# Kernel tuning notes

Measured on AMD Instinct MI355X. Metric: run time of the kernel, lower is better.

The kernel has to match this reference:

```python
import jax, jax.numpy as jnp
import numpy as np

E = 64      # embedding_dim
H = 64      # h_dim
MLP = 1024  # mlp_dim (attention hidden)
PRE1 = 512  # mlp_pre_pool hidden
BNK = 1024  # bottleneck_dim
S = 256     # num scenes (equal-size groups replacing seq_start_end)
P = 16      # pedestrians per scene
B = S * P   # total batch of pedestrians
T = 8       # obs_len for vx/vy (only last row used)
EPS = 1e-5  # BatchNorm eps


def _bn(x, g, b, m, v):
    # eval-mode BatchNorm1d over the last (feature) axis
    return (x - m) * jax.lax.rsqrt(v + EPS) * g + b


def setup_inputs() -> dict:
    key = jax.random.key(0)
    ks = jax.random.split(key, 24)
    def n(k, shape, s=1.0):
        return jax.random.normal(k, shape, jnp.float32) * s
    return {
        "h_states": n(ks[0], (1, B, H)),
        "end_pos": n(ks[1], (B, 2)),
        "vx": n(ks[2], (T, B)),
        "vy": n(ks[3], (T, B)),
        "W_sp": n(ks[4], (2, E), 0.05), "b_sp": jnp.zeros((E,), jnp.float32),
        "W_vel": n(ks[5], (2, E), 0.05), "b_vel": jnp.zeros((E,), jnp.float32),
        "Wa1": n(ks[6], (2 * E, MLP), 0.05), "ba1": jnp.zeros((MLP,), jnp.float32),
        "ga1": jnp.ones((MLP,), jnp.float32), "bta1": jnp.zeros((MLP,), jnp.float32),
        "ma1": n(ks[7], (MLP,), 0.1), "va1": jax.random.uniform(ks[8], (MLP,), jnp.float32) + 0.5,
        "Wa2": n(ks[9], (MLP, 1), 0.05), "ba2": jnp.zeros((1,), jnp.float32),
        "ga2": jnp.ones((1,), jnp.float32), "bta2": jnp.zeros((1,), jnp.float32),
        "ma2": n(ks[10], (1,), 0.1), "va2": jax.random.uniform(ks[11], (1,), jnp.float32) + 0.5,
        "Wp1": n(ks[12], (E + H, PRE1), 0.05), "bp1": jnp.zeros((PRE1,), jnp.float32),
        "gp1": jnp.ones((PRE1,), jnp.float32), "btp1": jnp.zeros((PRE1,), jnp.float32),
        "mp1": n(ks[13], (PRE1,), 0.1), "vp1": jax.random.uniform(ks[14], (PRE1,), jnp.float32) + 0.5,
        "Wp2": n(ks[15], (PRE1, BNK), 0.05), "bp2": jnp.zeros((BNK,), jnp.float32),
        "gp2": jnp.ones((BNK,), jnp.float32), "btp2": jnp.zeros((BNK,), jnp.float32),
        "mp2": n(ks[16], (BNK,), 0.1), "vp2": jax.random.uniform(ks[17], (BNK,), jnp.float32) + 0.5,
        "num_scenes": S, "num_ped": P,
    }


def _forward(h_states, end_pos, vx, vy, W_sp, b_sp, W_vel, b_vel,
             Wa1, ba1, ga1, bta1, ma1, va1, Wa2, ba2, ga2, bta2, ma2, va2,
             Wp1, bp1, gp1, btp1, mp1, vp1, Wp2, bp2, gp2, btp2, mp2, vp2,
             num_scenes, num_ped):
    Sn, Pn = num_scenes, num_ped
    h = h_states.reshape(-1, H).reshape(Sn, Pn, H)          # per-scene hidden
    pos = end_pos.reshape(Sn, Pn, 2)
    # rel[s,i,j] = pos[s,j] - pos[s,i]  (repeat vs repeat_interleave in torch)
    rel = pos[:, None, :, :] - pos[:, :, None, :]
    rel_emb = rel @ W_sp + b_sp                              # [S,P,P,E]
    vel = jnp.stack([vx[-1], vy[-1]], axis=-1).reshape(Sn, Pn, 2)
    vel_emb = vel @ W_vel + b_vel                            # [S,P,E], indexed by row i
    vel_emb = jnp.broadcast_to(vel_emb[:, :, None, :], (Sn, Pn, Pn, E))
    att_in = jnp.concatenate([rel_emb, vel_emb], axis=-1)    # [S,P,P,2E]
    a = jax.nn.relu(_bn(att_in @ Wa1 + ba1, ga1, bta1, ma1, va1))
    scores = jax.nn.relu(_bn(a @ Wa2 + ba2, ga2, bta2, ma2, va2))  # [S,P,P,1]
    # torch.softmax(scores, dim=1) on an (N,1) tensor: softmax over the size-1
    # feature axis -> identically 1.0. Reproduced faithfully here.
    w = jax.nn.softmax(scores, axis=-1)
    h_rep = jnp.broadcast_to(h[:, None, :, :], (Sn, Pn, Pn, H))   # h[s,j] per (i,j)
    x = jnp.concatenate([rel_emb, h_rep], axis=-1) * (0.05 * w)   # [S,P,P,E+H]
    y = jax.nn.relu(_bn(x @ Wp1 + bp1, gp1, btp1, mp1, vp1))
    y = jax.nn.relu(_bn(y @ Wp2 + bp2, gp2, btp2, mp2, vp2))      # [S,P,P,BNK]
    pool = jnp.max(y, axis=2)                                     # max over neighbors j
    return pool.reshape(Sn * Pn, BNK)


def reference(h_states, end_pos, vx, vy, W_sp, b_sp, W_vel, b_vel,
              Wa1, ba1, ga1, bta1, ma1, va1, Wa2, ba2, ga2, bta2, ma2, va2,
              Wp1, bp1, gp1, btp1, mp1, vp1, Wp2, bp2, gp2, btp2, mp2, vp2,
              num_scenes, num_ped):
    return _forward(h_states, end_pos, vx, vy, W_sp, b_sp, W_vel, b_vel,
                    Wa1, ba1, ga1, bta1, ma1, va1, Wa2, ba2, ga2, bta2, ma2, va2,
                    Wp1, bp1, gp1, btp1, mp1, vp1, Wp2, bp2, gp2, btp2, mp2, vp2,
                    num_scenes, num_ped)
```

## Files before the change

kernel.cpp:

```cpp
#include <hip/hip_runtime.h>
#include <hip/hip_bf16.h>
#include <stdint.h>
#include <utility>


typedef __bf16 bf16x8 __attribute__((ext_vector_type(8)));
typedef __bf16 bf16x2 __attribute__((ext_vector_type(2)));
typedef float  f32x4  __attribute__((ext_vector_type(4)));
typedef float  f32x2  __attribute__((ext_vector_type(2)));
typedef float  f32x16 __attribute__((ext_vector_type(16)));

#define BP2_OFF 0u
#define BP1_OFF 1048576u
#define MX_OFF  1114112u
#define MY_OFF  1116160u
#define CB_OFF  1118208u
#define SH_OFF  1120256u
#define A2_OFF  1122304u
#define C2_OFF  1126400u

#define Y1_LDS  0
#define HH_LDS  131072
#define LDS_SZ  147456

__device__ __forceinline__ unsigned short f2bf(float f) {
    union { float f; unsigned u; } c; c.f = f;
    unsigned u = c.u;
    return (unsigned short)((u + 0x7fffu + ((u >> 16) & 1u)) >> 16);
}
__device__ __forceinline__ float bfbits2f(unsigned hi) {
    union { unsigned u; float f; } c; c.u = hi; return c.f;
}
__device__ __forceinline__ unsigned pk_bf16(float a, float b) {
#if __has_builtin(__builtin_amdgcn_cvt_pk_bf16_f32)
    bf16x2 p = __builtin_amdgcn_cvt_pk_bf16_f32(a, b);
    union { bf16x2 v; unsigned u; } c; c.v = p; return c.u;
#else
    return (unsigned)f2bf(a) | ((unsigned)f2bf(b) << 16);
#endif
}
__device__ __forceinline__ int y1off(int r, int c16) {
    return r * 1024 + ((c16 ^ (r & 7)) << 4);
}

template<class F, int... Is>
__device__ __forceinline__ void sf_impl(F& f, std::integer_sequence<int, Is...>) {
    (f(std::integral_constant<int, Is>{}), ...);
}
template<int N, class F>
__device__ __forceinline__ void static_for(F&& f) {
    sf_impl(f, std::make_integer_sequence<int, N>{});
}

__global__ __launch_bounds__(256) void prep_pack_kernel(
    const float* __restrict__ Wsp,  const float* __restrict__ bsp,
    const float* __restrict__ Wp1,  const float* __restrict__ bp1,
    const float* __restrict__ gp1,  const float* __restrict__ btp1,
    const float* __restrict__ mp1,  const float* __restrict__ vp1,
    const float* __restrict__ Wp2,  const float* __restrict__ bp2,
    const float* __restrict__ gp2,  const float* __restrict__ btp2,
    const float* __restrict__ mp2,  const float* __restrict__ vp2,
    unsigned char* __restrict__ ws)
{
    __shared__ float tile[32 * 65];
    __shared__ float part[3][4][64];
    const int blk = blockIdx.x, t = threadIdx.x;

    if (blk < 272) {
        const float* src; int ncols, kb, ng;
        if (blk < 256) { kb = blk >> 4; ng = blk & 15; src = Wp2; ncols = 1024; }
        else { int b2 = blk - 256; kb = b2 >> 3; ng = b2 & 7; src = Wp1 + 64 * 512; ncols = 512; }
        const int k0 = kb * 32, n0 = ng * 64;
        #pragma unroll
        for (int it = 0; it < 2; ++it) {
            int c = t + it * 256;
            int r = c >> 4, c4 = c & 15;
            float4 v = *(const float4*)(src + (k0 + r) * ncols + n0 + c4 * 4);
            tile[r * 65 + c4 * 4 + 0] = v.x;
            tile[r * 65 + c4 * 4 + 1] = v.y;
            tile[r * 65 + c4 * 4 + 2] = v.z;
            tile[r * 65 + c4 * 4 + 3] = v.w;
        }
        __syncthreads();
        if (blk < 256) {
            const int l = t & 63, ch = (t >> 6) & 1, kh = t >> 7;
            const int nl = ch * 32 + (l & 31);
            const int kl = kh * 16 + ((l >> 5) & 1) * 8;
            uint4 o;
            o.x = pk_bf16(tile[(kl + 0) * 65 + nl], tile[(kl + 1) * 65 + nl]);
            o.y = pk_bf16(tile[(kl + 2) * 65 + nl], tile[(kl + 3) * 65 + nl]);
            o.z = pk_bf16(tile[(kl + 4) * 65 + nl], tile[(kl + 5) * 65 + nl]);
            o.w = pk_bf16(tile[(kl + 6) * 65 + nl], tile[(kl + 7) * 65 + nl]);
            const int kstep = kb * 2 + kh, ct = ng * 2 + ch;
            ((uint4*)(ws + BP2_OFF))[(kstep * 32 + ct) * 64 + l] = o;
        } else {
            int ntl = t >> 6, l = t & 63;
            int nl = ntl * 16 + (l & 15), kl = (l >> 4) * 8;
            uint4 o;
            o.x = pk_bf16(tile[(kl + 0) * 65 + nl], tile[(kl + 1) * 65 + nl]);
            o.y = pk_bf16(tile[(kl + 2) * 65 + nl], tile[(kl + 3) * 65 + nl]);
            o.z = pk_bf16(tile[(kl + 4) * 65 + nl], tile[(kl + 5) * 65 + nl]);
            o.w = pk_bf16(tile[(kl + 6) * 65 + nl], tile[(kl + 7) * 65 + nl]);
            ((uint4*)(ws + BP1_OFF))[((ng * 4 + ntl) * 2 + kb) * 64 + l] = o;
        }
    } else if (blk < 280) {
        const int kk = t & 63, eq = t >> 6;
        const int k = (blk - 272) * 64 + kk;
        float mx = 0.f, my = 0.f, cb = 0.f;
        #pragma unroll
        for (int e2 = 0; e2 < 16; ++e2) {
            int e = eq * 16 + e2;
            float wv = Wp1[e * 512 + k];
            mx = fmaf(Wsp[e],      wv, mx);
            my = fmaf(Wsp[64 + e], wv, my);
            cb = fmaf(bsp[e],      wv, cb);
        }
        part[0][eq][kk] = mx; part[1][eq][kk] = my; part[2][eq][kk] = cb;
        __syncthreads();
        if (t < 64) {
            const int k2 = (blk - 272) * 64 + t;
            float mxs = part[0][0][t] + part[0][1][t] + part[0][2][t] + part[0][3][t];
            float mys = part[1][0][t] + part[1][1][t] + part[1][2][t] + part[1][3][t];
            float cbs = part[2][0][t] + part[2][1][t] + part[2][2][t] + part[2][3][t];
            float a1 = gp1[k2] * rsqrtf(vp1[k2] + 1e-5f);
            ((float*)(ws + MX_OFF))[k2] = 0.05f * a1 * mxs;
            ((float*)(ws + MY_OFF))[k2] = 0.05f * a1 * mys;
            ((float*)(ws + CB_OFF))[k2] = 0.05f * a1 * cbs + (bp1[k2] - mp1[k2]) * a1 + btp1[k2];
            ((float*)(ws + SH_OFF))[k2] = 0.05f * a1;
        }
    } else {
        int n = (blk - 280) * 256 + t;
        float a = gp2[n] * rsqrtf(vp2[n] + 1e-5f);
        ((float*)(ws + A2_OFF))[n] = a;
        ((float*)(ws + C2_OFF))[n] = btp2[n] + (bp2[n] - mp2[n]) * a;
    }
}

__device__ __forceinline__ void phaseAB(
    unsigned char* smem,
    const float* __restrict__ hst, const float* __restrict__ epos,
    const unsigned char* __restrict__ ws, int s, int ih, int tid)
{
    const int w    = tid >> 6;
    const int l    = tid & 63;
    const int quad = l >> 4;
    const int jl   = l & 15;

    {
        union { unsigned u[4]; bf16x8 v; } afh[2];
        #pragma unroll
        for (int kb = 0; kb < 2; ++kb) {
            const float4* hp = (const float4*)(hst + (s * 16 + jl) * 64 + kb * 32 + quad * 8);
            float4 v0 = hp[0], v1 = hp[1];
            afh[kb].u[0] = pk_bf16(v0.x, v0.y);
            afh[kb].u[1] = pk_bf16(v0.z, v0.w);
            afh[kb].u[2] = pk_bf16(v1.x, v1.y);
            afh[kb].u[3] = pk_bf16(v1.z, v1.w);
        }
        const f32x4 fz = {0.f, 0.f, 0.f, 0.f};
        f32x4 acch[4] = {fz, fz, fz, fz};
        #pragma unroll
        for (int kb = 0; kb < 2; ++kb) {
            #pragma unroll
            for (int ct = 0; ct < 4; ++ct) {
                bf16x8 bfr = *(const bf16x8*)(ws + BP1_OFF + ((((w * 4 + ct) * 2 + kb) * 64 + l) << 4));
                acch[ct] = __builtin_amdgcn_mfma_f32_16x16x32_bf16(afh[kb].v, bfr, acch[ct], 0, 0, 0);
            }
        }
        const float* SHg = (const float*)(ws + SH_OFF);
        const float* CBg = (const float*)(ws + CB_OFF);
        #pragma unroll
        for (int ct = 0; ct < 4; ++ct) {
            int col = (w * 4 + ct) * 16 + jl;
            float sh = SHg[col], cb = CBg[col];
            #pragma unroll
            for (int reg = 0; reg < 4; ++reg) {
                int j = quad * 4 + reg;
                float hv = fmaf(acch[ct][reg], sh, cb);
                *(unsigned short*)(smem + HH_LDS + j * 1024 + col * 2) = f2bf(hv);
            }
        }
    }
    __syncthreads();

    {
        const int i2 = tid >> 8;
        const int j  = (tid >> 4) & 15;
        const int kc = tid & 15;
        float rx[4], ry[4];
        float pjx = epos[s * 32 + j * 2], pjy = epos[s * 32 + j * 2 + 1];
        #pragma unroll
        for (int ii = 0; ii < 4; ++ii) {
            int ig_ = ih * 8 + i2 * 4 + ii;
            rx[ii] = pjx - epos[s * 32 + ig_ * 2];
            ry[ii] = pjy - epos[s * 32 + ig_ * 2 + 1];
        }
        const f32x2 zero2 = {0.f, 0.f};
        #pragma unroll
        for (int kk = 0; kk < 4; ++kk) {
            int c16 = kk * 16 + kc;
            int k = c16 * 8;
            uint4 hh8 = *(const uint4*)(smem + HH_LDS + j * 1024 + k * 2);
            f32x4 mx0 = *(const f32x4*)(ws + MX_OFF + k * 4);
            f32x4 mx1 = *(const f32x4*)(ws + MX_OFF + k * 4 + 16);
            f32x4 my0 = *(const f32x4*)(ws + MY_OFF + k * 4);
            f32x4 my1 = *(const f32x4*)(ws + MY_OFF + k * 4 + 16);
            f32x2 mxp[4] = { {mx0[0],mx0[1]}, {mx0[2],mx0[3]}, {mx1[0],mx1[1]}, {mx1[2],mx1[3]} };
            f32x2 myp[4] = { {my0[0],my0[1]}, {my0[2],my0[3]}, {my1[0],my1[1]}, {my1[2],my1[3]} };
            f32x2 hhp[4];
            hhp[0][0] = bfbits2f(hh8.x << 16); hhp[0][1] = bfbits2f(hh8.x & 0xffff0000u);
            hhp[1][0] = bfbits2f(hh8.y << 16); hhp[1][1] = bfbits2f(hh8.y & 0xffff0000u);
            hhp[2][0] = bfbits2f(hh8.z << 16); hhp[2][1] = bfbits2f(hh8.z & 0xffff0000u);
            hhp[3][0] = bfbits2f(hh8.w << 16); hhp[3][1] = bfbits2f(hh8.w & 0xffff0000u);
            #pragma unroll
            for (int ii = 0; ii < 4; ++ii) {
                f32x2 rx2 = { rx[ii], rx[ii] };
                f32x2 ry2 = { ry[ii], ry[ii] };
                uint4 o;
                unsigned uu[4];
                #pragma unroll
                for (int p = 0; p < 4; ++p) {
                    f32x2 tt = __builtin_elementwise_fma(ry2, myp[p], hhp[p]);
                    tt = __builtin_elementwise_fma(rx2, mxp[p], tt);
                    tt = __builtin_elementwise_max(tt, zero2);
                    uu[p] = pk_bf16(tt[0], tt[1]);
                }
                o.x = uu[0]; o.y = uu[1]; o.z = uu[2]; o.w = uu[3];
                int r = (i2 * 4 + ii) * 16 + j;
                *(uint4*)(smem + Y1_LDS + y1off(r, c16)) = o;
            }
        }
    }
    __syncthreads();
}

__global__ __launch_bounds__(512, 2) void mm2_kernel(
    const float* __restrict__ hst,
    const float* __restrict__ epos,
    const unsigned char* __restrict__ ws,
    float* __restrict__ out)
{
    __shared__ __align__(16) unsigned char smem[LDS_SZ];

    const int s   = blockIdx.x >> 1;
    const int ih  = blockIdx.x & 1;
    const int tid = threadIdx.x;

    phaseAB(smem, hst, epos, ws, s, ih, tid);

    const int w = tid >> 6, l = tid & 63;
    const int lane31 = l & 31;
    const int hi = l >> 5;
    const int sr = lane31 & 7;
    const int rg = w >> 2;
    const int cg = w & 3;
    const float* A2 = (const float*)(ws + A2_OFF);
    const float* C2 = (const float*)(ws + C2_OFF);

    const int av = Y1_LDS + (rg * 64 + lane31) * 1024 + ((hi ^ sr) << 4);
    const unsigned char* bp = ws + BP2_OFF + ((cg * 4) << 10) + (l << 4);

    const f32x16 fz16 = {0.f,0.f,0.f,0.f,0.f,0.f,0.f,0.f,
                         0.f,0.f,0.f,0.f,0.f,0.f,0.f,0.f};
    f32x16 acc[2][4];
    bf16x8 ar[4][2];
    bf16x8 br[3][4];

    #pragma unroll
    for (int rr = 0; rr < 2; ++rr)
        #pragma unroll
        for (int c = 0; c < 4; ++c) acc[rr][c] = fz16;

    auto epilogue = [&](int pass) {
        #pragma unroll
        for (int c = 0; c < 4; ++c) {
            const int col = (pass * 16 + cg * 4 + c) * 32 + lane31;
            const float a2 = A2[col], c2 = C2[col];
            #pragma unroll
            for (int rr = 0; rr < 2; ++rr) {
                float mv[2];
                #pragma unroll
                for (int hg = 0; hg < 2; ++hg) {
                    float v0 = fmaxf(fmaf(acc[rr][c][hg * 8 + 0], a2, c2), 0.f);
                    float v1 = fmaxf(fmaf(acc[rr][c][hg * 8 + 1], a2, c2), 0.f);
                    float v2 = fmaxf(fmaf(acc[rr][c][hg * 8 + 2], a2, c2), 0.f);
                    float v3 = fmaxf(fmaf(acc[rr][c][hg * 8 + 3], a2, c2), 0.f);
                    float v4 = fmaxf(fmaf(acc[rr][c][hg * 8 + 4], a2, c2), 0.f);
                    float v5 = fmaxf(fmaf(acc[rr][c][hg * 8 + 5], a2, c2), 0.f);
                    float v6 = fmaxf(fmaf(acc[rr][c][hg * 8 + 6], a2, c2), 0.f);
                    float v7 = fmaxf(fmaf(acc[rr][c][hg * 8 + 7], a2, c2), 0.f);
                    float m = fmaxf(fmaxf(fmaxf(v0, v1), fmaxf(v2, v3)),
                                    fmaxf(fmaxf(v4, v5), fmaxf(v6, v7)));
                    mv[hg] = fmaxf(m, __shfl_xor(m, 32, 64));
                }
                const int iloc = (rg * 2 + rr) * 2 + hi;
                const float vout = hi ? mv[1] : mv[0];
                const int orow = s * 16 + ih * 8 + iloc;
                __builtin_nontemporal_store(vout, &out[orow * 1024 + col]);
            }
        }
    };

    auto stepG = [&](auto Gc) {
        constexpr int G  = decltype(Gc)::value;
        constexpr int GN = G + 2;
        if constexpr (GN <= 63) {
            constexpr int pn = GN >> 5, kn = GN & 31;
            constexpr int bs = GN % 3, as = GN & 3;
            const unsigned char* b = bp + (pn * 16384 + kn * 32768);
            #pragma unroll
            for (int c = 0; c < 4; ++c)
                br[bs][c] = *(const bf16x8*)(b + c * 1024);
            constexpr int add = (kn >> 2) * 128;
            constexpr int xr  = (kn & 3) << 5;
            ar[as][0] = *(const bf16x8*)(smem + ((av + add) ^ xr));
            ar[as][1] = *(const bf16x8*)(smem + (((av + add) ^ xr) + 32768));
        }
        if constexpr (G == 32 || G == 33)
            asm volatile("s_waitcnt vmcnt(16) lgkmcnt(4)" ::: "memory");
        else if constexpr (G == 62)
            asm volatile("s_waitcnt vmcnt(4) lgkmcnt(2)" ::: "memory");
        else if constexpr (G == 63)
            asm volatile("s_waitcnt vmcnt(0) lgkmcnt(0)" ::: "memory");
        else
            asm volatile("s_waitcnt vmcnt(8) lgkmcnt(4)" ::: "memory");
        __builtin_amdgcn_sched_barrier(0);
        constexpr int as2 = G & 3, bs2 = G % 3;
        #pragma unroll
        for (int c = 0; c < 4; ++c)
            #pragma unroll
            for (int rr = 0; rr < 2; ++rr)
                acc[rr][c] = __builtin_amdgcn_mfma_f32_32x32x16_bf16(
                    ar[as2][rr], br[bs2][c], acc[rr][c], 0, 0, 0);
    };

    #pragma unroll
    for (int g = 0; g < 2; ++g)
        #pragma unroll
        for (int c = 0; c < 4; ++c)
            br[g][c] = *(const bf16x8*)(bp + g * 32768 + c * 1024);
    ar[0][0] = *(const bf16x8*)(smem + av);
    ar[0][1] = *(const bf16x8*)(smem + av + 32768);
    ar[1][0] = *(const bf16x8*)(smem + (av ^ 32));
    ar[1][1] = *(const bf16x8*)(smem + ((av ^ 32) + 32768));

    static_for<32>(stepG);
    __builtin_amdgcn_sched_barrier(0);
    epilogue(0);
    #pragma unroll
    for (int rr = 0; rr < 2; ++rr)
        #pragma unroll
        for (int c = 0; c < 4; ++c) acc[rr][c] = fz16;
    __builtin_amdgcn_sched_barrier(0);
    static_for<32>([&](auto kc) {
        stepG(std::integral_constant<int, decltype(kc)::value + 32>{});
    });
    __builtin_amdgcn_sched_barrier(0);
    epilogue(1);
}

extern "C" void kernel_launch(void* const* d_in, const int* in_sizes, int n_in,
                              void* d_out, int out_size, void* d_ws, size_t ws_size,
                              hipStream_t stream) {
    const float* hst  = (const float*)d_in[0];
    const float* epos = (const float*)d_in[1];
    const float* Wsp  = (const float*)d_in[4];
    const float* bsp  = (const float*)d_in[5];
    const float* Wp1  = (const float*)d_in[20];
    const float* bp1  = (const float*)d_in[21];
    const float* gp1  = (const float*)d_in[22];
    const float* btp1 = (const float*)d_in[23];
    const float* mp1  = (const float*)d_in[24];
    const float* vp1  = (const float*)d_in[25];
    const float* Wp2  = (const float*)d_in[26];
    const float* bp2  = (const float*)d_in[27];
    const float* gp2  = (const float*)d_in[28];
    const float* btp2 = (const float*)d_in[29];
    const float* mp2  = (const float*)d_in[30];
    const float* vp2  = (const float*)d_in[31];
    unsigned char* ws = (unsigned char*)d_ws;
    float* out = (float*)d_out;

    prep_pack_kernel<<<284, 256, 0, stream>>>(Wsp, bsp, Wp1, bp1, gp1, btp1, mp1, vp1,
                                              Wp2, bp2, gp2, btp2, mp2, vp2, ws);
    mm2_kernel<<<512, 512, 0, stream>>>(hst, epos, ws, out);
}
```

Measured before the change: 186.8 us.

## Split each scene into four 4-row blocks of 256 threads instead of two

```diff
diff --git a/kernel.cpp b/kernel.cpp
--- a/kernel.cpp
+++ b/kernel.cpp
@@ -20,8 +20,8 @@
 #define C2_OFF  1126400u
 
 #define Y1_LDS  0
-#define HH_LDS  131072
-#define LDS_SZ  147456
+#define HH_LDS  65536
+#define LDS_SZ  81920
 
 __device__ __forceinline__ unsigned short f2bf(float f) {
     union { float f; unsigned u; } c; c.f = f;
@@ -136,11 +136,17 @@
     }
 }
 
-__device__ __forceinline__ void phaseAB(
-    unsigned char* smem,
-    const float* __restrict__ hst, const float* __restrict__ epos,
-    const unsigned char* __restrict__ ws, int s, int ih, int tid)
+__global__ __launch_bounds__(256, 2) void mm3_kernel(
+    const float* __restrict__ hst,
+    const float* __restrict__ epos,
+    const unsigned char* __restrict__ ws,
+    float* __restrict__ out)
 {
+    __shared__ __align__(16) unsigned char smem[LDS_SZ];
+
+    const int s   = blockIdx.x >> 2;
+    const int q   = blockIdx.x & 3;
+    const int tid = threadIdx.x;
     const int w    = tid >> 6;
     const int l    = tid & 63;
     const int quad = l >> 4;
@@ -158,20 +164,20 @@
             afh[kb].u[3] = pk_bf16(v1.z, v1.w);
         }
         const f32x4 fz = {0.f, 0.f, 0.f, 0.f};
-        f32x4 acch[4] = {fz, fz, fz, fz};
+        f32x4 acch[8] = {fz, fz, fz, fz, fz, fz, fz, fz};
         #pragma unroll
         for (int kb = 0; kb < 2; ++kb) {
             #pragma unroll
-            for (int ct = 0; ct < 4; ++ct) {
-                bf16x8 bfr = *(const bf16x8*)(ws + BP1_OFF + ((((w * 4 + ct) * 2 + kb) * 64 + l) << 4));
+            for (int ct = 0; ct < 8; ++ct) {
+                bf16x8 bfr = *(const bf16x8*)(ws + BP1_OFF + ((((w * 8 + ct) * 2 + kb) * 64 + l) << 4));
                 acch[ct] = __builtin_amdgcn_mfma_f32_16x16x32_bf16(afh[kb].v, bfr, acch[ct], 0, 0, 0);
             }
         }
         const float* SHg = (const float*)(ws + SH_OFF);
         const float* CBg = (const float*)(ws + CB_OFF);
         #pragma unroll
-        for (int ct = 0; ct < 4; ++ct) {
-            int col = (w * 4 + ct) * 16 + jl;
+        for (int ct = 0; ct < 8; ++ct) {
+            int col = (w * 8 + ct) * 16 + jl;
             float sh = SHg[col], cb = CBg[col];
             #pragma unroll
             for (int reg = 0; reg < 4; ++reg) {
@@ -184,14 +190,13 @@
     __syncthreads();
 
     {
-        const int i2 = tid >> 8;
-        const int j  = (tid >> 4) & 15;
+        const int j  = tid >> 4;
         const int kc = tid & 15;
         float rx[4], ry[4];
         float pjx = epos[s * 32 + j * 2], pjy = epos[s * 32 + j * 2 + 1];
         #pragma unroll
         for (int ii = 0; ii < 4; ++ii) {
-            int ig_ = ih * 8 + i2 * 4 + ii;
+            int ig_ = q * 4 + ii;
             rx[ii] = pjx - epos[s * 32 + ig_ * 2];
             ry[ii] = pjy - epos[s * 32 + ig_ * 2 + 1];
         }
@@ -226,137 +231,121 @@
                     uu[p] = pk_bf16(tt[0], tt[1]);
                 }
                 o.x = uu[0]; o.y = uu[1]; o.z = uu[2]; o.w = uu[3];
-                int r = (i2 * 4 + ii) * 16 + j;
+                int r = ii * 16 + j;
                 *(uint4*)(smem + Y1_LDS + y1off(r, c16)) = o;
             }
         }
     }
     __syncthreads();
-}
-
-__global__ __launch_bounds__(512, 2) void mm2_kernel(
-    const float* __restrict__ hst,
-    const float* __restrict__ epos,
-    const unsigned char* __restrict__ ws,
-    float* __restrict__ out)
-{
-    __shared__ __align__(16) unsigned char smem[LDS_SZ];
-
-    const int s   = blockIdx.x >> 1;
-    const int ih  = blockIdx.x & 1;
-    const int tid = threadIdx.x;
-
-    phaseAB(smem, hst, epos, ws, s, ih, tid);
-
-    const int w = tid >> 6, l = tid & 63;
-    const int lane31 = l & 31;
-    const int hi = l >> 5;
-    const int sr = lane31 & 7;
-    const int rg = w >> 2;
-    const int cg = w & 3;
-    const float* A2 = (const float*)(ws + A2_OFF);
-    const float* C2 = (const float*)(ws + C2_OFF);
-
-    const int av = Y1_LDS + (rg * 64 + lane31) * 1024 + ((hi ^ sr) << 4);
-    const unsigned char* bp = ws + BP2_OFF + ((cg * 4) << 10) + (l << 4);
-
-    const f32x16 fz16 = {0.f,0.f,0.f,0.f,0.f,0.f,0.f,0.f,
-                         0.f,0.f,0.f,0.f,0.f,0.f,0.f,0.f};
-    f32x16 acc[2][4];
-    bf16x8 ar[4][2];
-    bf16x8 br[3][4];
-
-    #pragma unroll
-    for (int rr = 0; rr < 2; ++rr)
-        #pragma unroll
-        for (int c = 0; c < 4; ++c) acc[rr][c] = fz16;
-
-    auto epilogue = [&](int pass) {
-        #pragma unroll
-        for (int c = 0; c < 4; ++c) {
-            const int col = (pass * 16 + cg * 4 + c) * 32 + lane31;
-            const float a2 = A2[col], c2 = C2[col];
-            #pragma unroll
-            for (int rr = 0; rr < 2; ++rr) {
-                float mv[2];
+
+    {
+        const int lane31 = l & 31;
+        const int hi = l >> 5;
+        const int sr = lane31 & 7;
+        const float* A2 = (const float*)(ws + A2_OFF);
+        const float* C2 = (const float*)(ws + C2_OFF);
+
+        const int av = Y1_LDS + lane31 * 1024 + ((hi ^ sr) << 4);
+        const unsigned char* bp = ws + BP2_OFF + ((w * 4) << 10) + (l << 4);
+
+        const f32x16 fz16 = {0.f,0.f,0.f,0.f,0.f,0.f,0.f,0.f,
+                             0.f,0.f,0.f,0.f,0.f,0.f,0.f,0.f};
+        f32x16 acc[2][4];
+        bf16x8 ar[4][2];
+        bf16x8 br[3][4];
+
+        #pragma unroll
+        for (int rr = 0; rr < 2; ++rr)
+            #pragma unroll
+            for (int c = 0; c < 4; ++c) acc[rr][c] = fz16;
+
+        auto epilogue = [&](int pass) {
+            #pragma unroll
+            for (int c = 0; c < 4; ++c) {
+                const int col = (pass * 16 + w * 4 + c) * 32 + lane31;
+                const float a2 = A2[col], c2 = C2[col];
                 #pragma unroll
-                for (int hg = 0; hg < 2; ++hg) {
-                    float v0 = fmaxf(fmaf(acc[rr][c][hg * 8 + 0], a2, c2), 0.f);
-                    float v1 = fmaxf(fmaf(acc[rr][c][hg * 8 + 1], a2, c2), 0.f);
-                    float v2 = fmaxf(fmaf(acc[rr][c][hg * 8 + 2], a2, c2), 0.f);
-                    float v3 = fmaxf(fmaf(acc[rr][c][hg * 8 + 3], a2, c2), 0.f);
-                    float v4 = fmaxf(fmaf(acc[rr][c][hg * 8 + 4], a2, c2), 0.f);
-                    float v5 = fmaxf(fmaf(acc[rr][c][hg * 8 + 5], a2, c2), 0.f);
-                    float v6 = fmaxf(fmaf(acc[rr][c][hg * 8 + 6], a2, c2), 0.f);
-                    float v7 = fmaxf(fmaf(acc[rr][c][hg * 8 + 7], a2, c2), 0.f);
-                    float m = fmaxf(fmaxf(fmaxf(v0, v1), fmaxf(v2, v3)),
-                                    fmaxf(fmaxf(v4, v5), fmaxf(v6, v7)));
-                    mv[hg] = fmaxf(m, __shfl_xor(m, 32, 64));
+                for (int rr = 0; rr < 2; ++rr) {
+                    float mv[2];
+                    #pragma unroll
+                    for (int hg = 0; hg < 2; ++hg) {
+                        float v0 = fmaxf(fmaf(acc[rr][c][hg * 8 + 0], a2, c2), 0.f);
+                        float v1 = fmaxf(fmaf(acc[rr][c][hg * 8 + 1], a2, c2), 0.f);
+                        float v2 = fmaxf(fmaf(acc[rr][c][hg * 8 + 2], a2, c2), 0.f);
+                        float v3 = fmaxf(fmaf(acc[rr][c][hg * 8 + 3], a2, c2), 0.f);
+                        float v4 = fmaxf(fmaf(acc[rr][c][hg * 8 + 4], a2, c2), 0.f);
+                        float v5 = fmaxf(fmaf(acc[rr][c][hg * 8 + 5], a2, c2), 0.f);
+                        float v6 = fmaxf(fmaf(acc[rr][c][hg * 8 + 6], a2, c2), 0.f);
+                        float v7 = fmaxf(fmaf(acc[rr][c][hg * 8 + 7], a2, c2), 0.f);
+                        float m = fmaxf(fmaxf(fmaxf(v0, v1), fmaxf(v2, v3)),
+                                        fmaxf(fmaxf(v4, v5), fmaxf(v6, v7)));
+                        mv[hg] = fmaxf(m, __shfl_xor(m, 32, 64));
+                    }
+                    const int iloc = rr * 2 + hi;
+                    const float vout = hi ? mv[1] : mv[0];
+                    const int orow = s * 16 + q * 4 + iloc;
+                    __builtin_nontemporal_store(vout, &out[orow * 1024 + col]);
                 }
-                const int iloc = (rg * 2 + rr) * 2 + hi;
-                const float vout = hi ? mv[1] : mv[0];
-                const int orow = s * 16 + ih * 8 + iloc;
-                __builtin_nontemporal_store(vout, &out[orow * 1024 + col]);
-            }
-        }
-    };
-
-    auto stepG = [&](auto Gc) {
-        constexpr int G  = decltype(Gc)::value;
-        constexpr int GN = G + 2;
-        if constexpr (GN <= 63) {
-            constexpr int pn = GN >> 5, kn = GN & 31;
-            constexpr int bs = GN % 3, as = GN & 3;
-            const unsigned char* b = bp + (pn * 16384 + kn * 32768);
+            }
+        };
+
+        auto stepG = [&](auto Gc) {
+            constexpr int G  = decltype(Gc)::value;
+            constexpr int GN = G + 2;
+            if constexpr (GN <= 63) {
+                constexpr int pn = GN >> 5, kn = GN & 31;
+                constexpr int bs = GN % 3, as = GN & 3;
+                const unsigned char* b = bp + (pn * 16384 + kn * 32768);
+                #pragma unroll
+                for (int c = 0; c < 4; ++c)
+                    br[bs][c] = *(const bf16x8*)(b + c * 1024);
+                constexpr int add = (kn >> 2) * 128;
+                constexpr int xr  = (kn & 3) << 5;
+                ar[as][0] = *(const bf16x8*)(smem + ((av + add) ^ xr));
+                ar[as][1] = *(const bf16x8*)(smem + (((av + add) ^ xr) + 32768));
+            }
+            if constexpr (G == 32 || G == 33)
+                asm volatile("s_waitcnt vmcnt(16) lgkmcnt(4)" ::: "memory");
+            else if constexpr (G == 62)
+                asm volatile("s_waitcnt vmcnt(4) lgkmcnt(2)" ::: "memory");
+            else if constexpr (G == 63)
+                asm volatile("s_waitcnt vmcnt(0) lgkmcnt(0)" ::: "memory");
+            else
+                asm volatile("s_waitcnt vmcnt(8) lgkmcnt(4)" ::: "memory");
+            __builtin_amdgcn_sched_barrier(0);
+            constexpr int as2 = G & 3, bs2 = G % 3;
             #pragma unroll
             for (int c = 0; c < 4; ++c)
-                br[bs][c] = *(const bf16x8*)(b + c * 1024);
-            constexpr int add = (kn >> 2) * 128;
-            constexpr int xr  = (kn & 3) << 5;
-            ar[as][0] = *(const bf16x8*)(smem + ((av + add) ^ xr));
-            ar[as][1] = *(const bf16x8*)(smem + (((av + add) ^ xr) + 32768));
-        }
-        if constexpr (G == 32 || G == 33)
-            asm volatile("s_waitcnt vmcnt(16) lgkmcnt(4)" ::: "memory");
-        else if constexpr (G == 62)
-            asm volatile("s_waitcnt vmcnt(4) lgkmcnt(2)" ::: "memory");
-        else if constexpr (G == 63)
-            asm volatile("s_waitcnt vmcnt(0) lgkmcnt(0)" ::: "memory");
-        else
-            asm volatile("s_waitcnt vmcnt(8) lgkmcnt(4)" ::: "memory");
+                #pragma unroll
+                for (int rr = 0; rr < 2; ++rr)
+                    acc[rr][c] = __builtin_amdgcn_mfma_f32_32x32x16_bf16(
+                        ar[as2][rr], br[bs2][c], acc[rr][c], 0, 0, 0);
+        };
+
+        #pragma unroll
+        for (int g = 0; g < 2; ++g)
+            #pragma unroll
+            for (int c = 0; c < 4; ++c)
+                br[g][c] = *(const bf16x8*)(bp + g * 32768 + c * 1024);
+        ar[0][0] = *(const bf16x8*)(smem + av);
+        ar[0][1] = *(const bf16x8*)(smem + av + 32768);
+        ar[1][0] = *(const bf16x8*)(smem + (av ^ 32));
+        ar[1][1] = *(const bf16x8*)(smem + ((av ^ 32) + 32768));
+
+        static_for<32>(stepG);
         __builtin_amdgcn_sched_barrier(0);
-        constexpr int as2 = G & 3, bs2 = G % 3;
-        #pragma unroll
-        for (int c = 0; c < 4; ++c)
-            #pragma unroll
-            for (int rr = 0; rr < 2; ++rr)
-                acc[rr][c] = __builtin_amdgcn_mfma_f32_32x32x16_bf16(
-                    ar[as2][rr], br[bs2][c], acc[rr][c], 0, 0, 0);
-    };
-
-    #pragma unroll
-    for (int g = 0; g < 2; ++g)
-        #pragma unroll
-        for (int c = 0; c < 4; ++c)
-            br[g][c] = *(const bf16x8*)(bp + g * 32768 + c * 1024);
-    ar[0][0] = *(const bf16x8*)(smem + av);
-    ar[0][1] = *(const bf16x8*)(smem + av + 32768);
-    ar[1][0] = *(const bf16x8*)(smem + (av ^ 32));
-    ar[1][1] = *(const bf16x8*)(smem + ((av ^ 32) + 32768));
-
-    static_for<32>(stepG);
-    __builtin_amdgcn_sched_barrier(0);
-    epilogue(0);
-    #pragma unroll
-    for (int rr = 0; rr < 2; ++rr)
-        #pragma unroll
-        for (int c = 0; c < 4; ++c) acc[rr][c] = fz16;
-    __builtin_amdgcn_sched_barrier(0);
-    static_for<32>([&](auto kc) {
-        stepG(std::integral_constant<int, decltype(kc)::value + 32>{});
-    });
-    __builtin_amdgcn_sched_barrier(0);
-    epilogue(1);
+        epilogue(0);
+        #pragma unroll
+        for (int rr = 0; rr < 2; ++rr)
+            #pragma unroll
+            for (int c = 0; c < 4; ++c) acc[rr][c] = fz16;
+        __builtin_amdgcn_sched_barrier(0);
+        static_for<32>([&](auto kc) {
+            stepG(std::integral_constant<int, decltype(kc)::value + 32>{});
+        });
+        __builtin_amdgcn_sched_barrier(0);
+        epilogue(1);
+    }
 }
 
 extern "C" void kernel_launch(void* const* d_in, const int* in_sizes, int n_in,
@@ -383,5 +372,5 @@
 
     prep_pack_kernel<<<284, 256, 0, stream>>>(Wsp, bsp, Wp1, bp1, gp1, btp1, mp1, vp1,
                                               Wp2, bp2, gp2, btp2, mp2, vp2, ws);
-    mm2_kernel<<<512, 512, 0, stream>>>(hst, epos, ws, out);
-}
+    mm3_kernel<<<1024, 256, 0, stream>>>(hst, epos, ws, out);
+}
```

After: 188.0 us. No clear change (+0.6%).

## Split per-block work across 16 waves with smaller per-wave MFMA tiles

Applied to the files above, without the earlier changes.

```diff
diff --git a/kernel.cpp b/kernel.cpp
--- a/kernel.cpp
+++ b/kernel.cpp
@@ -22,6 +22,9 @@
 #define Y1_LDS  0
 #define HH_LDS  131072
 #define LDS_SZ  147456
+
+#define WAITCNT(S) do { asm volatile("s_waitcnt " S ::: "memory"); \
+                        __builtin_amdgcn_sched_barrier(0); } while (0)
 
 __device__ __forceinline__ unsigned short f2bf(float f) {
     union { float f; unsigned u; } c; c.f = f;
@@ -136,11 +139,17 @@
     }
 }
 
-__device__ __forceinline__ void phaseAB(
-    unsigned char* smem,
-    const float* __restrict__ hst, const float* __restrict__ epos,
-    const unsigned char* __restrict__ ws, int s, int ih, int tid)
+__global__ __launch_bounds__(1024, 4) void mm4_kernel(
+    const float* __restrict__ hst,
+    const float* __restrict__ epos,
+    const unsigned char* __restrict__ ws,
+    float* __restrict__ out)
 {
+    __shared__ __align__(16) unsigned char smem[LDS_SZ];
+
+    const int s   = blockIdx.x >> 1;
+    const int ih  = blockIdx.x & 1;
+    const int tid = threadIdx.x;
     const int w    = tid >> 6;
     const int l    = tid & 63;
     const int quad = l >> 4;
@@ -158,20 +167,20 @@
             afh[kb].u[3] = pk_bf16(v1.z, v1.w);
         }
         const f32x4 fz = {0.f, 0.f, 0.f, 0.f};
-        f32x4 acch[4] = {fz, fz, fz, fz};
+        f32x4 acch[2] = {fz, fz};
         #pragma unroll
         for (int kb = 0; kb < 2; ++kb) {
             #pragma unroll
-            for (int ct = 0; ct < 4; ++ct) {
-                bf16x8 bfr = *(const bf16x8*)(ws + BP1_OFF + ((((w * 4 + ct) * 2 + kb) * 64 + l) << 4));
+            for (int ct = 0; ct < 2; ++ct) {
+                bf16x8 bfr = *(const bf16x8*)(ws + BP1_OFF + ((((w * 2 + ct) * 2 + kb) * 64 + l) << 4));
                 acch[ct] = __builtin_amdgcn_mfma_f32_16x16x32_bf16(afh[kb].v, bfr, acch[ct], 0, 0, 0);
             }
         }
         const float* SHg = (const float*)(ws + SH_OFF);
         const float* CBg = (const float*)(ws + CB_OFF);
         #pragma unroll
-        for (int ct = 0; ct < 4; ++ct) {
-            int col = (w * 4 + ct) * 16 + jl;
+        for (int ct = 0; ct < 2; ++ct) {
+            int col = (w * 2 + ct) * 16 + jl;
             float sh = SHg[col], cb = CBg[col];
             #pragma unroll
             for (int reg = 0; reg < 4; ++reg) {
@@ -184,14 +193,14 @@
     __syncthreads();
 
     {
-        const int i2 = tid >> 8;
+        const int i4 = tid >> 8;
         const int j  = (tid >> 4) & 15;
         const int kc = tid & 15;
-        float rx[4], ry[4];
+        float rx[2], ry[2];
         float pjx = epos[s * 32 + j * 2], pjy = epos[s * 32 + j * 2 + 1];
         #pragma unroll
-        for (int ii = 0; ii < 4; ++ii) {
-            int ig_ = ih * 8 + i2 * 4 + ii;
+        for (int ii = 0; ii < 2; ++ii) {
+            int ig_ = ih * 8 + i4 * 2 + ii;
             rx[ii] = pjx - epos[s * 32 + ig_ * 2];
             ry[ii] = pjy - epos[s * 32 + ig_ * 2 + 1];
         }
@@ -213,7 +222,7 @@
             hhp[2][0] = bfbits2f(hh8.z << 16); hhp[2][1] = bfbits2f(hh8.z & 0xffff0000u);
             hhp[3][0] = bfbits2f(hh8.w << 16); hhp[3][1] = bfbits2f(hh8.w & 0xffff0000u);
             #pragma unroll
-            for (int ii = 0; ii < 4; ++ii) {
+            for (int ii = 0; ii < 2; ++ii) {
                 f32x2 rx2 = { rx[ii], rx[ii] };
                 f32x2 ry2 = { ry[ii], ry[ii] };
                 uint4 o;
@@ -226,137 +235,115 @@
                     uu[p] = pk_bf16(tt[0], tt[1]);
                 }
                 o.x = uu[0]; o.y = uu[1]; o.z = uu[2]; o.w = uu[3];
-                int r = (i2 * 4 + ii) * 16 + j;
+                int r = (i4 * 2 + ii) * 16 + j;
                 *(uint4*)(smem + Y1_LDS + y1off(r, c16)) = o;
             }
         }
     }
     __syncthreads();
-}
-
-__global__ __launch_bounds__(512, 2) void mm2_kernel(
-    const float* __restrict__ hst,
-    const float* __restrict__ epos,
-    const unsigned char* __restrict__ ws,
-    float* __restrict__ out)
-{
-    __shared__ __align__(16) unsigned char smem[LDS_SZ];
-
-    const int s   = blockIdx.x >> 1;
-    const int ih  = blockIdx.x & 1;
-    const int tid = threadIdx.x;
-
-    phaseAB(smem, hst, epos, ws, s, ih, tid);
-
-    const int w = tid >> 6, l = tid & 63;
-    const int lane31 = l & 31;
-    const int hi = l >> 5;
-    const int sr = lane31 & 7;
-    const int rg = w >> 2;
-    const int cg = w & 3;
-    const float* A2 = (const float*)(ws + A2_OFF);
-    const float* C2 = (const float*)(ws + C2_OFF);
-
-    const int av = Y1_LDS + (rg * 64 + lane31) * 1024 + ((hi ^ sr) << 4);
-    const unsigned char* bp = ws + BP2_OFF + ((cg * 4) << 10) + (l << 4);
-
-    const f32x16 fz16 = {0.f,0.f,0.f,0.f,0.f,0.f,0.f,0.f,
-                         0.f,0.f,0.f,0.f,0.f,0.f,0.f,0.f};
-    f32x16 acc[2][4];
-    bf16x8 ar[4][2];
-    bf16x8 br[3][4];
-
-    #pragma unroll
-    for (int rr = 0; rr < 2; ++rr)
-        #pragma unroll
-        for (int c = 0; c < 4; ++c) acc[rr][c] = fz16;
-
-    auto epilogue = [&](int pass) {
-        #pragma unroll
-        for (int c = 0; c < 4; ++c) {
-            const int col = (pass * 16 + cg * 4 + c) * 32 + lane31;
-            const float a2 = A2[col], c2 = C2[col];
-            #pragma unroll
-            for (int rr = 0; rr < 2; ++rr) {
-                float mv[2];
+
+    {
+        const int lane31 = l & 31;
+        const int hi = l >> 5;
+        const int sr = lane31 & 7;
+        const int rg = w >> 3;
+        const int cg = w & 7;
+        const float* A2 = (const float*)(ws + A2_OFF);
+        const float* C2 = (const float*)(ws + C2_OFF);
+
+        int av[2];
+        #pragma unroll
+        for (int rr = 0; rr < 2; ++rr)
+            av[rr] = Y1_LDS + ((rg * 2 + rr) * 32 + lane31) * 1024 + ((hi ^ sr) << 4);
+
+        const unsigned char* bp = ws + BP2_OFF + ((cg * 2) << 10) + (l << 4);
+
+        const f32x16 fz16 = {0.f,0.f,0.f,0.f,0.f,0.f,0.f,0.f,
+                             0.f,0.f,0.f,0.f,0.f,0.f,0.f,0.f};
+        f32x16 acc[2][2];
+        bf16x8 ar[2][2];
+        bf16x8 br[2][2];
+
+        #pragma unroll
+        for (int rr = 0; rr < 2; ++rr) { acc[rr][0] = fz16; acc[rr][1] = fz16; }
+
+        auto epilogue = [&](int pass) {
+            #pragma unroll
+            for (int c = 0; c < 2; ++c) {
+                const int col = (pass * 16 + cg * 2 + c) * 32 + lane31;
+                const float a2 = A2[col], c2 = C2[col];
                 #pragma unroll
-                for (int hg = 0; hg < 2; ++hg) {
-                    float v0 = fmaxf(fmaf(acc[rr][c][hg * 8 + 0], a2, c2), 0.f);
-                    float v1 = fmaxf(fmaf(acc[rr][c][hg * 8 + 1], a2, c2), 0.f);
-                    float v2 = fmaxf(fmaf(acc[rr][c][hg * 8 + 2], a2, c2), 0.f);
-                    float v3 = fmaxf(fmaf(acc[rr][c][hg * 8 + 3], a2, c2), 0.f);
-                    float v4 = fmaxf(fmaf(acc[rr][c][hg * 8 + 4], a2, c2), 0.f);
-                    float v5 = fmaxf(fmaf(acc[rr][c][hg * 8 + 5], a2, c2), 0.f);
-                    float v6 = fmaxf(fmaf(acc[rr][c][hg * 8 + 6], a2, c2), 0.f);
-                    float v7 = fmaxf(fmaf(acc[rr][c][hg * 8 + 7], a2, c2), 0.f);
-                    float m = fmaxf(fmaxf(fmaxf(v0, v1), fmaxf(v2, v3)),
-                                    fmaxf(fmaxf(v4, v5), fmaxf(v6, v7)));
-                    mv[hg] = fmaxf(m, __shfl_xor(m, 32, 64));
+                for (int rr = 0; rr < 2; ++rr) {
+                    float mv[2];
+                    #pragma unroll
+                    for (int hg = 0; hg < 2; ++hg) {
+                        float v0 = fmaxf(fmaf(acc[rr][c][hg * 8 + 0], a2, c2), 0.f);
+                        float v1 = fmaxf(fmaf(acc[rr][c][hg * 8 + 1], a2, c2), 0.f);
+                        float v2 = fmaxf(fmaf(acc[rr][c][hg * 8 + 2], a2, c2), 0.f);
+                        float v3 = fmaxf(fmaf(acc[rr][c][hg * 8 + 3], a2, c2), 0.f);
+                        float v4 = fmaxf(fmaf(acc[rr][c][hg * 8 + 4], a2, c2), 0.f);
+                        float v5 = fmaxf(fmaf(acc[rr][c][hg * 8 + 5], a2, c2), 0.f);
+                        float v6 = fmaxf(fmaf(acc[rr][c][hg * 8 + 6], a2, c2), 0.f);
+                        float v7 = fmaxf(fmaf(acc[rr][c][hg * 8 + 7], a2, c2), 0.f);
+                        float m = fmaxf(fmaxf(fmaxf(v0, v1), fmaxf(v2, v3)),
+                                        fmaxf(fmaxf(v4, v5), fmaxf(v6, v7)));
+                        mv[hg] = fmaxf(m, __shfl_xor(m, 32, 64));
+                    }
+                    const int iloc = (rg * 2 + rr) * 2 + hi;
+                    const float vout = hi ? mv[1] : mv[0];
+                    const int orow = s * 16 + ih * 8 + iloc;
+                    __builtin_nontemporal_store(vout, &out[orow * 1024 + col]);
                 }
-                const int iloc = (rg * 2 + rr) * 2 + hi;
-                const float vout = hi ? mv[1] : mv[0];
-                const int orow = s * 16 + ih * 8 + iloc;
-                __builtin_nontemporal_store(vout, &out[orow * 1024 + col]);
             }
-        }
-    };
-
-    auto stepG = [&](auto Gc) {
-        constexpr int G  = decltype(Gc)::value;
-        constexpr int GN = G + 2;
-        if constexpr (GN <= 63) {
-            constexpr int pn = GN >> 5, kn = GN & 31;
-            constexpr int bs = GN % 3, as = GN & 3;
+        };
+
+        auto issueG = [&](auto Gc) {
+            constexpr int GN = decltype(Gc)::value;
+            constexpr int pn = GN >> 5, kn = GN & 31, sl = GN & 1;
             const unsigned char* b = bp + (pn * 16384 + kn * 32768);
-            #pragma unroll
-            for (int c = 0; c < 4; ++c)
-                br[bs][c] = *(const bf16x8*)(b + c * 1024);
+            br[sl][0] = *(const bf16x8*)(b);
+            br[sl][1] = *(const bf16x8*)(b + 1024);
             constexpr int add = (kn >> 2) * 128;
             constexpr int xr  = (kn & 3) << 5;
-            ar[as][0] = *(const bf16x8*)(smem + ((av + add) ^ xr));
-            ar[as][1] = *(const bf16x8*)(smem + (((av + add) ^ xr) + 32768));
-        }
-        if constexpr (G == 32 || G == 33)
-            asm volatile("s_waitcnt vmcnt(16) lgkmcnt(4)" ::: "memory");
-        else if constexpr (G == 62)
-            asm volatile("s_waitcnt vmcnt(4) lgkmcnt(2)" ::: "memory");
-        else if constexpr (G == 63)
-            asm volatile("s_waitcnt vmcnt(0) lgkmcnt(0)" ::: "memory");
-        else
-            asm volatile("s_waitcnt vmcnt(8) lgkmcnt(4)" ::: "memory");
+            #pragma unroll
+            for (int rr = 0; rr < 2; ++rr)
+                ar[sl][rr] = *(const bf16x8*)(smem + ((av[rr] + add) ^ xr));
+        };
+
+        auto stepG = [&](auto Gc) {
+            constexpr int G = decltype(Gc)::value;
+            if constexpr (G + 1 <= 63)
+                issueG(std::integral_constant<int, G + 1>{});
+            if constexpr (G == 32)
+                asm volatile("s_waitcnt vmcnt(10) lgkmcnt(2)" ::: "memory");
+            else if constexpr (G == 63)
+                asm volatile("s_waitcnt vmcnt(0) lgkmcnt(0)" ::: "memory");
+            else
+                asm volatile("s_waitcnt vmcnt(2) lgkmcnt(2)" ::: "memory");
+            __builtin_amdgcn_sched_barrier(0);
+            constexpr int sl = G & 1;
+            #pragma unroll
+            for (int c = 0; c < 2; ++c)
+                #pragma unroll
+                for (int rr = 0; rr < 2; ++rr)
+                    acc[rr][c] = __builtin_amdgcn_mfma_f32_32x32x16_bf16(
+                        ar[sl][rr], br[sl][c], acc[rr][c], 0, 0, 0);
+        };
+
+        issueG(std::integral_constant<int, 0>{});
+
+        static_for<32>(stepG);
         __builtin_amdgcn_sched_barrier(0);
-        constexpr int as2 = G & 3, bs2 = G % 3;
-        #pragma unroll
-        for (int c = 0; c < 4; ++c)
-            #pragma unroll
-            for (int rr = 0; rr < 2; ++rr)
-                acc[rr][c] = __builtin_amdgcn_mfma_f32_32x32x16_bf16(
-                    ar[as2][rr], br[bs2][c], acc[rr][c], 0, 0, 0);
-    };
-
-    #pragma unroll
-    for (int g = 0; g < 2; ++g)
-        #pragma unroll
-        for (int c = 0; c < 4; ++c)
-            br[g][c] = *(const bf16x8*)(bp + g * 32768 + c * 1024);
-    ar[0][0] = *(const bf16x8*)(smem + av);
-    ar[0][1] = *(const bf16x8*)(smem + av + 32768);
-    ar[1][0] = *(const bf16x8*)(smem + (av ^ 32));
-    ar[1][1] = *(const bf16x8*)(smem + ((av ^ 32) + 32768));
-
-    static_for<32>(stepG);
-    __builtin_amdgcn_sched_barrier(0);
-    epilogue(0);
-    #pragma unroll
-    for (int rr = 0; rr < 2; ++rr)
-        #pragma unroll
-        for (int c = 0; c < 4; ++c) acc[rr][c] = fz16;
-    __builtin_amdgcn_sched_barrier(0);
-    static_for<32>([&](auto kc) {
-        stepG(std::integral_constant<int, decltype(kc)::value + 32>{});
-    });
-    __builtin_amdgcn_sched_barrier(0);
-    epilogue(1);
+        epilogue(0);
+        #pragma unroll
+        for (int rr = 0; rr < 2; ++rr) { acc[rr][0] = fz16; acc[rr][1] = fz16; }
+        __builtin_amdgcn_sched_barrier(0);
+        static_for<32>([&](auto kc) {
+            stepG(std::integral_constant<int, decltype(kc)::value + 32>{});
+        });
+        __builtin_amdgcn_sched_barrier(0);
+        epilogue(1);
+    }
 }
 
 extern "C" void kernel_launch(void* const* d_in, const int* in_sizes, int n_in,
@@ -383,5 +370,5 @@
 
     prep_pack_kernel<<<284, 256, 0, stream>>>(Wsp, bsp, Wp1, bp1, gp1, btp1, mp1, vp1,
                                               Wp2, bp2, gp2, btp2, mp2, vp2, ws);
-    mm2_kernel<<<512, 512, 0, stream>>>(hst, epos, ws, out);
-}
+    mm4_kernel<<<512, 1024, 0, stream>>>(hst, epos, ws, out);
+}
```

New measurement: 191.9 us. 2.7% more time.
